# Kernel optimization log

Hardware: AMD Instinct MI355X
Metric: run time of the kernel (lower is better)

## Reference

```python
import jax, jax.numpy as jnp
import numpy as np

S, B, C, H, E, V, T = 196, 64, 1024, 1024, 512, 32000, 20


def setup_inputs() -> dict:
    key = jax.random.key(0)
    ks = jax.random.split(key, 16)

    def w(k, shape, fan_in):
        return (jax.random.normal(k, shape, jnp.float32) / np.sqrt(fan_in)).astype(jnp.float32)

    emb_W = w(ks[2], (V, E), E).at[0].set(0.0)  # padding_idx=0
    return {
        'ctx': jax.random.normal(ks[0], (S, B, C), jnp.float32),
        'y': jax.random.randint(ks[1], (T, B), 0, V, jnp.int32),
        'emb_W': emb_W,
        'att_ctx2ctx': w(ks[3], (C, C), C),
        'att_hid2ctx': w(ks[4], (H, C), H),
        'att_mlp': w(ks[5], (C,), C),
        'gru_W_ih': w(ks[6], (3 * H, E + C), E + C),
        'gru_b_ih': jnp.zeros((3 * H,), jnp.float32),
        'gru_W_hh': w(ks[7], (3 * H, H), H),
        'gru_b_hh': jnp.zeros((3 * H,), jnp.float32),
        'hid2out_W': w(ks[8], (E, H), H),
        'hid2out_b': jnp.zeros((E,), jnp.float32),
        'out_ctx_W': w(ks[9], (E, C), C),
        'out_ctx_b': jnp.zeros((E,), jnp.float32),
        'out2prob_W': w(ks[10], (V, E), E),
        'out2prob_b': jnp.zeros((V,), jnp.float32),
    }


def reference(ctx, y, emb_W, att_ctx2ctx, att_hid2ctx, att_mlp,
              gru_W_ih, gru_b_ih, gru_W_hh, gru_b_hh,
              hid2out_W, hid2out_b, out_ctx_W, out_ctx_b,
              out2prob_W, out2prob_b):
    hidden = gru_W_hh.shape[1]
    y_emb = emb_W[y]                                        # [T, B, E]
    ctx_proj = jnp.einsum('sbc,cm->sbm', ctx, att_ctx2ctx)  # precompute ctx2ctx(ctx)

    def gru_cell(x, h):
        gi = x @ gru_W_ih.T + gru_b_ih
        gh = h @ gru_W_hh.T + gru_b_hh
        i_r, i_z, i_n = jnp.split(gi, 3, axis=-1)
        h_r, h_z, h_n = jnp.split(gh, 3, axis=-1)
        r = jax.nn.sigmoid(i_r + h_r)
        z = jax.nn.sigmoid(i_z + h_z)
        n = jnp.tanh(i_n + r * h_n)
        return (1.0 - z) * n + z * h

    def step(h, inp):
        y_t, tgt = inp                                      # [B,E], [B]
        # MLP attention over source positions S
        scores = jnp.einsum('sbm,m->sb', jnp.tanh(ctx_proj + (h @ att_hid2ctx)[None]), att_mlp)
        alpha = jax.nn.softmax(scores, axis=0)              # [S, B]
        z_t = jnp.einsum('sb,sbc->bc', alpha, ctx)          # [B, C]
        ht = gru_cell(jnp.concatenate([y_t, z_t], axis=-1), h)
        logit = jnp.tanh(ht @ hid2out_W.T + hid2out_b)      # hid2out (tanh FF)
        logit = logit + y_t                                 # prev2out
        logit = logit + z_t @ out_ctx_W.T + out_ctx_b       # ctx2out
        log_p = jax.nn.log_softmax(jnp.tanh(logit) @ out2prob_W.T + out2prob_b, axis=-1)
        mask = (tgt != 0).astype(log_p.dtype)               # NLLLoss ignore_index=0, sum
        nll = -jnp.sum(jnp.take_along_axis(log_p, tgt[:, None], axis=1)[:, 0] * mask)
        return ht, nll

    h0 = jnp.zeros((y.shape[1], hidden), ctx.dtype)         # dec_init='zero'
    _, nlls = jax.lax.scan(step, h0, (y_emb[:-1], y[1:]))
    return jnp.sum(nlls)
```

## Files before the change

### kernel.cpp

```cpp
#include <hip/hip_runtime.h>
#include <math.h>

#define TS_ 19

typedef float f32x4 __attribute__((ext_vector_type(4)));
typedef short s16x8 __attribute__((ext_vector_type(8)));
typedef unsigned short us;
typedef unsigned char uc;

__device__ __forceinline__ float sigmoidf_(float x) { return 1.f / (1.f + __expf(-x)); }

__device__ __forceinline__ float fast_tanh(float x) {
    float ax = fabsf(x);
    float e = __expf(-2.f * ax);
    float r = (1.f - e) * __builtin_amdgcn_rcpf(1.f + e);
    return copysignf(r, x);
}

__device__ __forceinline__ us f2b(float x) {
    union { float f; unsigned u; } v; v.f = x;
    unsigned r = v.u + 0x7fffu + ((v.u >> 16) & 1u);
    return (us)(r >> 16);
}
__device__ __forceinline__ float b2f(us u) {
    union { unsigned u; float f; } v; v.u = ((unsigned)u) << 16; return v.f;
}
__device__ __forceinline__ uc f2e4m3(float x) {
    return (uc)(__builtin_amdgcn_cvt_pk_fp8_f32(x, 0.f, 0, false) & 0xff);
}

#define MFMA(a, b, c) __builtin_amdgcn_mfma_f32_16x16x32_bf16((a), (b), (c), 0, 0, 0)
#define MFMA8(a, b, c) __builtin_amdgcn_mfma_f32_16x16x32_fp8_fp8((a), (b), (c), 0, 0, 0)

__device__ __forceinline__ f32x4 zero4() { return (f32x4){0.f, 0.f, 0.f, 0.f}; }

__device__ __forceinline__ f32x4 wg16(const us* ap, const us* bp, int nk, f32x4 acc) {
#pragma unroll 4
    for (int k = 0; k < nk; k += 32)
        acc = MFMA(*(const s16x8*)(ap + k), *(const s16x8*)(bp + k), acc);
    return acc;
}

__device__ __forceinline__ void gload_lds16(const void* g, void* l) {
    __builtin_amdgcn_global_load_lds(
        (const __attribute__((address_space(1))) unsigned int*)g,
        (__attribute__((address_space(3))) unsigned int*)l, 16, 0, 0);
}

__global__ __launch_bounds__(256) void k_prep(
    const float* __restrict__ ctx, us* __restrict__ ctxbf,
    const float* __restrict__ o2pW, uc* __restrict__ o2p8,
    const float* __restrict__ Wih, const float* __restrict__ Whh, us* __restrict__ Wg,
    const float* __restrict__ h2oW, us* __restrict__ h2obf,
    const float* __restrict__ octxW, us* __restrict__ octxbf,
    const float* __restrict__ att_c2c, us* __restrict__ c2cT,
    const float* __restrict__ att_h2c, us* __restrict__ attbf,
    const int* __restrict__ y, const float* __restrict__ embW, us* __restrict__ xc,
    float* __restrict__ hf32, us* __restrict__ ht_all,
    us* __restrict__ obf_all, uc* __restrict__ obf8, float* __restrict__ out) {
    __shared__ float tile[32][33];
    int bid = blockIdx.x, tid = threadIdx.x;
    const int4 z4 = {0, 0, 0, 0};

    if (bid < 1024) {
        for (long i = ((long)bid * 256 + tid) * 4; i < 12845056L; i += 1048576L) {
            float4 v = *(const float4*)(ctx + i);
            ushort4 o = { f2b(v.x), f2b(v.y), f2b(v.z), f2b(v.w) };
            *(ushort4*)(ctxbf + i) = o;
        }
    } else if (bid < 1792) {
        for (long i = ((long)(bid - 1024) * 256 + tid) * 8; i < 16384000L;
             i += 1572864L) {
            float4 v0 = *(const float4*)(o2pW + i);
            float4 v1 = *(const float4*)(o2pW + i + 4);
            int lo = __builtin_amdgcn_cvt_pk_fp8_f32(v0.x, v0.y, 0, false);
            lo = __builtin_amdgcn_cvt_pk_fp8_f32(v0.z, v0.w, lo, true);
            int hi = __builtin_amdgcn_cvt_pk_fp8_f32(v1.x, v1.y, 0, false);
            hi = __builtin_amdgcn_cvt_pk_fp8_f32(v1.z, v1.w, hi, true);
            int2 o = { lo, hi };
            *(int2*)(o2p8 + i) = o;
        }
    } else if (bid < 2816) {
        for (int n = bid - 1792; n < 4096; n += 1024) {
            int cl = n >> 10;
            if (cl < 2) {
                long bb = (long)n * 2560;
                const float* wi = Wih + (long)n * 1536;
                const float* wh = Whh + (long)n * 1024;
                for (int k = tid; k < 1536; k += 256) Wg[bb + k] = f2b(wi[k]);
                for (int k = tid; k < 1024; k += 256) Wg[bb + 1536 + k] = f2b(wh[k]);
            } else if (cl == 2) {
                long bb = 5242880L + (long)(n - 2048) * 1536;
                const float* wi = Wih + (long)n * 1536;
                for (int k = tid; k < 1536; k += 256) Wg[bb + k] = f2b(wi[k]);
            } else {
                long bb = 6815744L + (long)(n - 3072) * 1024;
                const float* wh = Whh + (long)(n - 1024) * 1024;
                for (int k = tid; k < 1024; k += 256) Wg[bb + k] = f2b(wh[k]);
            }
        }
    } else if (bid < 2880) {
        for (long i = ((long)(bid - 2816) * 256 + tid) * 4; i < 524288L; i += 65536L) {
            float4 v = *(const float4*)(h2oW + i);
            ushort4 o = { f2b(v.x), f2b(v.y), f2b(v.z), f2b(v.w) };
            *(ushort4*)(h2obf + i) = o;
        }
    } else if (bid < 2944) {
        for (long i = ((long)(bid - 2880) * 256 + tid) * 4; i < 524288L; i += 65536L) {
            float4 v = *(const float4*)(octxW + i);
            ushort4 o = { f2b(v.x), f2b(v.y), f2b(v.z), f2b(v.w) };
            *(ushort4*)(octxbf + i) = o;
        }
    } else if (bid < 3072) {
        for (int r = bid - 2944; r < 1216; r += 128) {
            int row = y[r];
            const float* src = embW + (long)row * 512;
            us* dst = xc + (long)r * 2560;
            for (int e = tid; e < 512; e += 256) dst[e] = f2b(src[e]);
        }
    } else if (bid < 4096) {
        int g = bid - 3072;
        int bx = (g & 31) * 32, by = (g >> 5) * 32;
        int x = tid & 31, y0 = tid >> 5;
        for (int yy = y0; yy < 32; yy += 8) tile[yy][x] = att_c2c[(by + yy) * 1024 + bx + x];
        __syncthreads();
        for (int yy = y0; yy < 32; yy += 8) c2cT[(bx + yy) * 1024 + by + x] = f2b(tile[x][yy]);
    } else if (bid < 5120) {
        int g = bid - 4096;
        int bx = (g & 31) * 32, by = (g >> 5) * 32;
        int x = tid & 31, y0 = tid >> 5;
        for (int yy = y0; yy < 32; yy += 8) tile[yy][x] = att_h2c[(by + yy) * 1024 + bx + x];
        __syncthreads();
        for (int yy = y0; yy < 32; yy += 8) attbf[(bx + yy) * 1024 + by + x] = f2b(tile[x][yy]);
    } else {
        int zb = bid - 5120;
        if (zb < 32) {
            int4* p = (int4*)hf32;
            int i = zb * 256 + tid;
            p[i] = z4; p[i + 8192] = z4;
        } else if (zb < 40) {
            int4* p = (int4*)ht_all;
            int i = (zb - 32) * 256 + tid;
#pragma unroll
            for (int k = 0; k < 4; ++k) p[i + k * 2048] = z4;
        } else if (zb < 56) {
            int cbase = (zb - 40) * 4;
#pragma unroll
            for (int c = 0; c < 4; ++c) {
                ushort4* p = (ushort4*)(xc + (long)(cbase + c) * 2560 + 1536);
                ushort4 o = {0, 0, 0, 0};
                p[tid] = o;
            }
        } else if (zb < 64) {
            int4* p = (int4*)(obf_all + 1216L * 512);
            int i = (zb - 56) * 256 + tid;
            p[i] = z4; p[i + 2048] = z4;
        } else if (zb < 68) {
            int4* p = (int4*)(obf8 + 1216L * 512);
            int i = (zb - 64) * 256 + tid;
            p[i] = z4; p[i + 1024] = z4;
        } else if (zb < 92) {
            int4* p = (int4*)(o2p8 + 16384000L);
            int i = (zb - 68) * 256 + tid;
#pragma unroll
            for (int k = 0; k < 4; ++k) p[i + k * 6144] = z4;
        } else {
            if (tid == 0) out[0] = 0.f;
        }
    }
}

__global__ __launch_bounds__(256) void k_gemm(const us* __restrict__ A,
                                              const us* __restrict__ Bt,
                                              us* __restrict__ Cb) {
    __shared__ us As[8192], Bs[8192];
    int tid = threadIdx.x, lane = tid & 63, w = tid >> 6;
    int mr = lane & 15, kb = lane >> 4;
    int bm = blockIdx.x % 98, bn = blockIdx.x / 98;
    long m0 = (long)bm * 128;
    int n0 = bn * 128;
    int wr = w >> 1, wc = w & 1;
    int srow = w * 32 + (lane >> 3);
    int ib = (lane & 7) * 16;

    f32x4 acc[4][4];
#pragma unroll
    for (int i = 0; i < 4; i++)
#pragma unroll
        for (int j = 0; j < 4; j++) acc[i][j] = zero4();

    for (int kt = 0; kt < 16; ++kt) {
        int k0 = kt * 64;
        __syncthreads();
#pragma unroll
        for (int c = 0; c < 4; ++c) {
            int r = srow + c * 8;
            int sw = (ib ^ ((r & 7) << 4)) >> 1;
            gload_lds16(A + (m0 + r) * 1024 + k0 + sw, &As[w * 2048 + c * 512]);
            gload_lds16(Bt + (long)(n0 + r) * 1024 + k0 + sw, &Bs[w * 2048 + c * 512]);
        }
        __syncthreads();
#pragma unroll
        for (int ks = 0; ks < 2; ++ks) {
            s16x8 af[4], bf[4];
#pragma unroll
            for (int mt = 0; mt < 4; ++mt) {
                int r = wr * 64 + mt * 16 + mr;
                af[mt] = *(const s16x8*)&As[(r * 128 + ((ks * 64 + kb * 16) ^ ((r & 7) << 4))) >> 1];
            }
#pragma unroll
            for (int nt = 0; nt < 4; ++nt) {
                int r = wc * 64 + nt * 16 + mr;
                bf[nt] = *(const s16x8*)&Bs[(r * 128 + ((ks * 64 + kb * 16) ^ ((r & 7) << 4))) >> 1];
            }
#pragma unroll
            for (int mt = 0; mt < 4; ++mt)
#pragma unroll
                for (int nt = 0; nt < 4; ++nt)
                    acc[mt][nt] = MFMA(af[mt], bf[nt], acc[mt][nt]);
        }
    }
#pragma unroll
    for (int mt = 0; mt < 4; ++mt)
#pragma unroll
        for (int nt = 0; nt < 4; ++nt)
#pragma unroll
            for (int j = 0; j < 4; ++j)
                Cb[(m0 + wr * 64 + mt * 16 + kb * 4 + j) * 1024 +
                   n0 + wc * 64 + nt * 16 + mr] = f2b(acc[mt][nt][j]);
}

__global__ __launch_bounds__(256) void k_hproj(const us* __restrict__ hcur,
                                               const us* __restrict__ attbf,
                                               float* __restrict__ hpp) {
    int tid = threadIdx.x, lane = tid & 63, w = tid >> 6;
    int vn0 = (blockIdx.x >> 1) * 16, kc = blockIdx.x & 1;
    int m0 = w * 16, mr = lane & 15, kb = lane >> 4;
    const us* ap = hcur + (long)(m0 + mr) * 1024 + kc * 512 + kb * 8;
    const us* bp = attbf + (long)(vn0 + mr) * 1024 + kc * 512 + kb * 8;
    f32x4 acc = wg16(ap, bp, 512, zero4());
#pragma unroll
    for (int j = 0; j < 4; ++j)
        hpp[(long)kc * 65536 + (long)(m0 + kb * 4 + j) * 1024 + vn0 + mr] = acc[j];
}

__global__ __launch_bounds__(1024) void k_scores(const us* __restrict__ cpb,
                                                 const float* __restrict__ hpp,
                                                 const float* __restrict__ mlp,
                                                 float* __restrict__ scores) {
    __shared__ float hp[1024];
    __shared__ float ml[1024];
    int tid = threadIdx.x;
    int b = blockIdx.x >> 2, sq = blockIdx.x & 3;
    hp[tid] = hpp[(long)b * 1024 + tid] + hpp[65536 + (long)b * 1024 + tid];
    ml[tid] = mlp[tid];
    __syncthreads();
    int wv = tid >> 6, lane = tid & 63;
    int s0 = sq * 49;
    for (int s = s0 + wv; s < s0 + 49; s += 16) {
        const us* cp = cpb + (long)(s * 64 + b) * 1024 + lane * 16;
        s16x8 c0 = *(const s16x8*)cp;
        s16x8 c1 = *(const s16x8*)(cp + 8);
        int e0 = lane * 16;
        float acc = 0.f;
#pragma unroll
        for (int j = 0; j < 8; ++j)
            acc += fast_tanh(b2f((us)c0[j]) + hp[e0 + j]) * ml[e0 + j];
#pragma unroll
        for (int j = 0; j < 8; ++j)
            acc += fast_tanh(b2f((us)c1[j]) + hp[e0 + 8 + j]) * ml[e0 + 8 + j];
#pragma unroll
        for (int off = 32; off; off >>= 1) acc += __shfl_xor(acc, off, 64);
        if (lane == 0) scores[b * 196 + s] = acc;
    }
}

__global__ __launch_bounds__(512) void k_z(const float* __restrict__ scores,
                                           const us* __restrict__ ctxbf,
                                           us* __restrict__ xc, int t) {
    __shared__ float red[512];
    __shared__ float als[196];
    __shared__ float zp[256];
    int tid = threadIdx.x, b = blockIdx.x >> 2, ch = blockIdx.x & 3;
    const float* sc = scores + b * 196;
    float lm = (tid < 196) ? sc[tid] : -1e30f;
    red[tid] = lm; __syncthreads();
    for (int st = 256; st; st >>= 1) { if (tid < st) red[tid] = fmaxf(red[tid], red[tid + st]); __syncthreads(); }
    float m = red[0]; __syncthreads();
    float ls = (tid < 196) ? __expf(sc[tid] - m) : 0.f;
    red[tid] = ls; __syncthreads();
    for (int st = 256; st; st >>= 1) { if (tid < st) red[tid] += red[tid + st]; __syncthreads(); }
    float inv = 1.f / red[0];
    if (tid < 196) als[tid] = ls * inv;
    __syncthreads();
    int c = ch * 256 + (tid & 255);
    int sh = tid >> 8;
    const us* cp = ctxbf + (long)b * 1024 + c;
    float a0 = 0.f;
    int sb = sh * 98;
#pragma unroll 4
    for (int s = sb; s < sb + 98; s += 2) {
        a0 += als[s] * b2f(cp[(long)s * 65536]) +
              als[s + 1] * b2f(cp[(long)(s + 1) * 65536]);
    }
    if (sh) zp[tid & 255] = a0;
    __syncthreads();
    if (!sh) {
        a0 += zp[tid & 255];
        xc[(long)(t * 64 + b) * 2560 + 512 + c] = f2b(a0);
    }
}

__global__ __launch_bounds__(512) void k_gruh2(us* __restrict__ xc,
                                               const us* __restrict__ Wg,
                                               const float* __restrict__ bih,
                                               const float* __restrict__ bhh,
                                               float* __restrict__ hf32,
                                               us* __restrict__ ht_all, int t) {
    __shared__ float lg[2048];
    int tid = threadIdx.x, lane = tid & 63, w = tid >> 6;
    int mr = lane & 15, kb = lane >> 4;
    int g = w >> 1, kh = w & 1;
    int xcd = blockIdx.x & 7, idx = blockIdx.x >> 3;
    int jt = xcd * 8 + (idx >> 2), mq = idx & 3;
    int m0 = mq * 16, j0 = jt * 16;
    const us* xr = xc + (long)t * 163840 + (long)(m0 + mr) * 2560;

    f32x4 acc = zero4();
    if (g == 0) {
        acc = wg16(xr + kh * 1280 + kb * 8,
                   Wg + (long)(j0 + mr) * 2560 + kh * 1280 + kb * 8, 1280, acc);
    } else if (g == 1) {
        acc = wg16(xr + kh * 1280 + kb * 8,
                   Wg + (long)(1024 + j0 + mr) * 2560 + kh * 1280 + kb * 8, 1280, acc);
    } else if (g == 2) {
        acc = wg16(xr + kh * 768 + kb * 8,
                   Wg + 5242880L + (long)(j0 + mr) * 1536 + kh * 768 + kb * 8, 768, acc);
    } else {
        acc = wg16(xr + 1536 + kh * 512 + kb * 8,
                   Wg + 6815744L + (long)(j0 + mr) * 1024 + kh * 512 + kb * 8, 512, acc);
    }
#pragma unroll
    for (int j = 0; j < 4; ++j)
        lg[(g * 2 + kh) * 256 + (kb * 4 + j) * 16 + mr] = acc[j];
    __syncthreads();

    if (tid < 256) {
        int ml = tid >> 4, jj = tid & 15;
        int b = m0 + ml, j = j0 + jj;
        float gr = lg[0 * 256 + ml * 16 + jj] + lg[1 * 256 + ml * 16 + jj];
        float gz = lg[2 * 256 + ml * 16 + jj] + lg[3 * 256 + ml * 16 + jj];
        float gi = lg[4 * 256 + ml * 16 + jj] + lg[5 * 256 + ml * 16 + jj];
        float gh = lg[6 * 256 + ml * 16 + jj] + lg[7 * 256 + ml * 16 + jj];
        float r  = sigmoidf_(gr + bih[j] + bhh[j]);
        float zz = sigmoidf_(gz + bih[1024 + j] + bhh[1024 + j]);
        float n  = fast_tanh(gi + bih[2048 + j] + r * (gh + bhh[2048 + j]));
        float h = (1.f - zz) * n + zz * hf32[b * 1024 + j];
        hf32[b * 1024 + j] = h;
        us hb = f2b(h);
        ht_all[(long)((t + 1) * 64 + b) * 1024 + j] = hb;
        if (t < TS_ - 1) xc[(long)((t + 1) * 64 + b) * 2560 + 1536 + j] = hb;
    }
}

__global__ __launch_bounds__(256) void k_outb(const us* __restrict__ ht_all,
                                              const us* __restrict__ xc,
                                              const us* __restrict__ h2obf,
                                              const float* __restrict__ h2ob,
                                              const us* __restrict__ octxbf,
                                              const float* __restrict__ octxb,
                                              us* __restrict__ obf_all,
                                              uc* __restrict__ obf8) {
    int tid = threadIdx.x, lane = tid & 63, w = tid >> 6;
    int mr = lane & 15, kb = lane >> 4;
    int m0 = blockIdx.x * 64;
    int n0 = blockIdx.y * 64;
    int e = n0 + w * 16 + mr;
    const us* bb1 = h2obf + (long)e * 1024 + kb * 8;
    const us* bb2 = octxbf + (long)e * 1024 + kb * 8;
    const us* ab1 = ht_all + (long)(64 + m0 + mr) * 1024 + kb * 8;
    const us* ab2 = xc + (long)(m0 + mr) * 2560 + 512 + kb * 8;

    f32x4 a1[4], a2[4];
#pragma unroll
    for (int i = 0; i < 4; i++) { a1[i] = zero4(); a2[i] = zero4(); }

#pragma unroll 2
    for (int k0 = 0; k0 < 1024; k0 += 32) {
        s16x8 b1 = *(const s16x8*)(bb1 + k0);
        s16x8 b2 = *(const s16x8*)(bb2 + k0);
#pragma unroll
        for (int mt = 0; mt < 4; ++mt) {
            a1[mt] = MFMA(*(const s16x8*)(ab1 + mt * 16384 + k0), b1, a1[mt]);
            a2[mt] = MFMA(*(const s16x8*)(ab2 + mt * 40960 + k0), b2, a2[mt]);
        }
    }
    float b1v = h2ob[e], b2v = octxb[e];
#pragma unroll
    for (int mt = 0; mt < 4; ++mt)
#pragma unroll
        for (int j = 0; j < 4; ++j) {
            long row = m0 + mt * 16 + kb * 4 + j;
            float ye = b2f(xc[row * 2560 + e]);
            float val = fast_tanh(fast_tanh(a1[mt][j] + b1v) + ye + a2[mt][j] + b2v);
            obf_all[(row << 9) + e] = f2b(val);
            obf8[(row << 9) + e] = f2e4m3(val);
        }
}

__global__ __launch_bounds__(256) void k_vocab8(const uc* __restrict__ obf8,
                                                const uc* __restrict__ o2p8,
                                                const float* __restrict__ o2pb,
                                                float* __restrict__ pm,
                                                float* __restrict__ ps) {
    __shared__ uc As[8192], Bs[8192];
    int tid = threadIdx.x, lane = tid & 63, w = tid >> 6;
    int mr = lane & 15, kb = lane >> 4;
    int xq = blockIdx.x & 7, idx = blockIdx.x >> 3;
    int nb = xq * 32 + idx / 10, mb = idx % 10;
    int m0 = mb * 128, n0 = nb * 128;
    int wr = w >> 1, wc = w & 1;
    int srow = w * 32 + (lane >> 2);
    int ib = (lane & 3) * 16;

    f32x4 acc[4][4];
#pragma unroll
    for (int i = 0; i < 4; i++)
#pragma unroll
        for (int j = 0; j < 4; j++) acc[i][j] = zero4();

    for (int kt = 0; kt < 8; ++kt) {
        int k0 = kt * 64;
        __syncthreads();
#pragma unroll
        for (int c = 0; c < 2; ++c) {
            int r = srow + c * 16;
            int sw = ib ^ ((r & 6) << 3);
            gload_lds16(obf8 + (long)(m0 + r) * 512 + k0 + sw, &As[w * 2048 + c * 1024]);
            gload_lds16(o2p8 + (long)(n0 + r) * 512 + k0 + sw, &Bs[w * 2048 + c * 1024]);
        }
        __syncthreads();
#pragma unroll
        for (int ks = 0; ks < 2; ++ks) {
            long af[4], bf[4];
#pragma unroll
            for (int mt = 0; mt < 4; ++mt) {
                int r = wr * 64 + mt * 16 + mr;
                af[mt] = *(const long*)&As[r * 64 + ((ks * 32 + kb * 8) ^ ((r & 6) << 3))];
            }
#pragma unroll
            for (int nt = 0; nt < 4; ++nt) {
                int r = wc * 64 + nt * 16 + mr;
                bf[nt] = *(const long*)&Bs[r * 64 + ((ks * 32 + kb * 8) ^ ((r & 6) << 3))];
            }
#pragma unroll
            for (int mt = 0; mt < 4; ++mt)
#pragma unroll
                for (int nt = 0; nt < 4; ++nt)
                    acc[mt][nt] = MFMA8(af[mt], bf[nt], acc[mt][nt]);
        }
    }

    int n0w = n0 + wc * 64;
    float bv[4];
#pragma unroll
    for (int nt = 0; nt < 4; ++nt) {
        int vn = n0w + nt * 16 + mr;
        bv[nt] = (vn < 32000) ? o2pb[vn] : -1e30f;
    }
#pragma unroll
    for (int mt = 0; mt < 4; ++mt)
#pragma unroll
        for (int j = 0; j < 4; ++j) {
            float x0 = acc[mt][0][j] + bv[0];
            float x1 = acc[mt][1][j] + bv[1];
            float x2 = acc[mt][2][j] + bv[2];
            float x3 = acc[mt][3][j] + bv[3];
            float m = fmaxf(fmaxf(x0, x1), fmaxf(x2, x3));
            float s = __expf(x0 - m) + __expf(x1 - m) + __expf(x2 - m) + __expf(x3 - m);
#pragma unroll
            for (int off = 1; off <= 8; off <<= 1) {
                float mo = __shfl_xor(m, off, 64), so = __shfl_xor(s, off, 64);
                float nm = fmaxf(m, mo);
                s = s * __expf(m - nm) + so * __expf(mo - nm);
                m = nm;
            }
            if (mr == 0) {
                int row = m0 + wr * 64 + mt * 16 + kb * 4 + j;
                pm[(long)(nb * 2 + wc) * 1280 + row] = m;
                ps[(long)(nb * 2 + wc) * 1280 + row] = s;
            }
        }
}

__global__ __launch_bounds__(64) void k_lseb(const float* __restrict__ pm,
                                             const float* __restrict__ ps,
                                             const us* __restrict__ obf_all,
                                             const float* __restrict__ o2pW,
                                             const float* __restrict__ o2pb,
                                             const int* __restrict__ y,
                                             float* __restrict__ out) {
    int r = blockIdx.x, lane = threadIdx.x;
    int t = r >> 6, b = r & 63;
    int tgt = y[(t + 1) * 64 + b];
    float m = -1e30f, s = 0.f;
    for (int p = lane; p < 512; p += 64) {
        float mi = pm[(long)p * 1280 + r], si = ps[(long)p * 1280 + r];
        float nm = fmaxf(m, mi);
        s = s * __expf(m - nm) + si * __expf(mi - nm);
        m = nm;
    }
#pragma unroll
    for (int off = 32; off; off >>= 1) {
        float mo = __shfl_xor(m, off, 64), so = __shfl_xor(s, off, 64);
        float nm = fmaxf(m, mo);
        s = s * __expf(m - nm) + so * __expf(mo - nm);
        m = nm;
    }
    float d = 0.f;
    const float* wr = o2pW + (long)tgt * 512;
#pragma unroll
    for (int k = 0; k < 8; ++k)
        d += b2f(obf_all[(long)r * 512 + lane + k * 64]) * wr[lane + k * 64];
#pragma unroll
    for (int off = 32; off; off >>= 1) d += __shfl_xor(d, off, 64);
    if (lane == 0 && tgt != 0)
        atomicAdd(out, (m + __logf(s)) - (d + o2pb[tgt]));
}

extern "C" void kernel_launch(void* const* d_in, const int* in_sizes, int n_in,
                              void* d_out, int out_size, void* d_ws, size_t ws_size,
                              hipStream_t stream) {
    const float* ctx     = (const float*)d_in[0];
    const int*   y       = (const int*)d_in[1];
    const float* embW    = (const float*)d_in[2];
    const float* att_c2c = (const float*)d_in[3];
    const float* att_h2c = (const float*)d_in[4];
    const float* mlp     = (const float*)d_in[5];
    const float* Wih     = (const float*)d_in[6];
    const float* bih     = (const float*)d_in[7];
    const float* Whh     = (const float*)d_in[8];
    const float* bhh     = (const float*)d_in[9];
    const float* h2oW    = (const float*)d_in[10];
    const float* h2ob    = (const float*)d_in[11];
    const float* octxW   = (const float*)d_in[12];
    const float* octxb   = (const float*)d_in[13];
    const float* o2pW    = (const float*)d_in[14];
    const float* o2pb    = (const float*)d_in[15];
    float* out = (float*)d_out;

    char* base = (char*)d_ws;
    us* ctxbf   = (us*)base; base += 25690112L;
    us* cpbf    = (us*)base; base += 25690112L;
    us* c2cT    = (us*)base; base += 2097152L;
    us* attbf   = (us*)base; base += 2097152L;
    us* Wg      = (us*)base; base += 15728640L;
    us* h2obf   = (us*)base; base += 1048576L;
    us* octxbf  = (us*)base; base += 1048576L;
    uc* o2p8    = (uc*)base; base += 16777216L;
    us* xc      = (us*)base; base += 6225920L;
    us* ht_all  = (us*)base; base += 2621440L;
    us* obf_all = (us*)base; base += 1310720L;
    uc* obf8    = (uc*)base; base += 655360L;
    float* hf32   = (float*)base; base += 262144L;
    float* hpp    = (float*)base; base += 524288L;
    float* scb    = (float*)base; base += 50176L;
    float* pm   = (float*)cpbf;
    float* ps   = pm + 655360L;

    k_prep<<<5213, 256, 0, stream>>>(ctx, ctxbf, o2pW, o2p8, Wih, Whh, Wg,
                                     h2oW, h2obf, octxW, octxbf,
                                     att_c2c, c2cT, att_h2c, attbf,
                                     y, embW, xc, hf32, ht_all, obf_all, obf8, out);
    k_gemm<<<784, 256, 0, stream>>>(ctxbf, c2cT, cpbf);

    for (int t = 0; t < TS_; t++) {
        k_hproj<<<128, 256, 0, stream>>>(ht_all + (long)t * 65536, attbf, hpp);
        k_scores<<<256, 1024, 0, stream>>>(cpbf, hpp, mlp, scb);
        k_z<<<256, 512, 0, stream>>>(scb, ctxbf, xc, t);
        k_gruh2<<<256, 512, 0, stream>>>(xc, Wg, bih, bhh, hf32, ht_all, t);
    }

    k_outb<<<dim3(19, 8), 256, 0, stream>>>(ht_all, xc, h2obf, h2ob, octxbf, octxb,
                                            obf_all, obf8);
    k_vocab8<<<2560, 256, 0, stream>>>(obf8, o2p8, o2pb, pm, ps);
    k_lseb<<<1216, 64, 0, stream>>>(pm, ps, obf_all, o2pW, o2pb, y, out);
}
```

Before: 982.7 us.

## Double-buffer LDS in fp8 vocab GEMM and vectorize GRU weight conversion

The fp8 vocab projection kernel now double-buffers its LDS tiles, prefetching the next K-slice with global_load_lds while MFMAs run on the current one, and uses one barrier per iteration instead of two. Separately, the GRU weight bf16 conversion in the prep kernel uses float4 vectorized loads and stores with half as many blocks, and the block ranges and grid size are shifted to match. The cost is doubled LDS use in the vocab kernel, which may reduce occupancy.

```diff
diff --git a/kernel.cpp b/kernel.cpp
--- a/kernel.cpp
+++ b/kernel.cpp
@@ -45,6 +45,12 @@
     __builtin_amdgcn_global_load_lds(
         (const __attribute__((address_space(1))) unsigned int*)g,
         (__attribute__((address_space(3))) unsigned int*)l, 16, 0, 0);
+}
+
+__device__ __forceinline__ void cvt4(const float* src, us* dst) {
+    float4 v = *(const float4*)src;
+    ushort4 o = { f2b(v.x), f2b(v.y), f2b(v.z), f2b(v.w) };
+    *(ushort4*)dst = o;
 }
 
 __global__ __launch_bounds__(256) void k_prep(
@@ -63,11 +69,8 @@
     const int4 z4 = {0, 0, 0, 0};
 
     if (bid < 1024) {
-        for (long i = ((long)bid * 256 + tid) * 4; i < 12845056L; i += 1048576L) {
-            float4 v = *(const float4*)(ctx + i);
-            ushort4 o = { f2b(v.x), f2b(v.y), f2b(v.z), f2b(v.w) };
-            *(ushort4*)(ctxbf + i) = o;
-        }
+        for (long i = ((long)bid * 256 + tid) * 4; i < 12845056L; i += 1048576L)
+            cvt4(ctx + i, ctxbf + i);
     } else if (bid < 1792) {
         for (long i = ((long)(bid - 1024) * 256 + tid) * 8; i < 16384000L;
              i += 1572864L) {
@@ -80,60 +83,55 @@
             int2 o = { lo, hi };
             *(int2*)(o2p8 + i) = o;
         }
-    } else if (bid < 2816) {
-        for (int n = bid - 1792; n < 4096; n += 1024) {
+    } else if (bid < 2304) {
+        for (int n = bid - 1792; n < 4096; n += 512) {
             int cl = n >> 10;
             if (cl < 2) {
-                long bb = (long)n * 2560;
+                us* wb = Wg + (long)n * 2560;
                 const float* wi = Wih + (long)n * 1536;
                 const float* wh = Whh + (long)n * 1024;
-                for (int k = tid; k < 1536; k += 256) Wg[bb + k] = f2b(wi[k]);
-                for (int k = tid; k < 1024; k += 256) Wg[bb + 1536 + k] = f2b(wh[k]);
+                for (int k4 = tid; k4 < 384; k4 += 256) cvt4(wi + k4 * 4, wb + k4 * 4);
+                if (tid < 256)
+                    cvt4(wh + tid * 4, wb + 1536 + tid * 4);
             } else if (cl == 2) {
-                long bb = 5242880L + (long)(n - 2048) * 1536;
+                us* wb = Wg + 5242880L + (long)(n - 2048) * 1536;
                 const float* wi = Wih + (long)n * 1536;
-                for (int k = tid; k < 1536; k += 256) Wg[bb + k] = f2b(wi[k]);
+                for (int k4 = tid; k4 < 384; k4 += 256) cvt4(wi + k4 * 4, wb + k4 * 4);
             } else {
-                long bb = 6815744L + (long)(n - 3072) * 1024;
+                us* wb = Wg + 6815744L + (long)(n - 3072) * 1024;
                 const float* wh = Whh + (long)(n - 1024) * 1024;
-                for (int k = tid; k < 1024; k += 256) Wg[bb + k] = f2b(wh[k]);
-            }
-        }
-    } else if (bid < 2880) {
-        for (long i = ((long)(bid - 2816) * 256 + tid) * 4; i < 524288L; i += 65536L) {
-            float4 v = *(const float4*)(h2oW + i);
-            ushort4 o = { f2b(v.x), f2b(v.y), f2b(v.z), f2b(v.w) };
-            *(ushort4*)(h2obf + i) = o;
-        }
-    } else if (bid < 2944) {
-        for (long i = ((long)(bid - 2880) * 256 + tid) * 4; i < 524288L; i += 65536L) {
-            float4 v = *(const float4*)(octxW + i);
-            ushort4 o = { f2b(v.x), f2b(v.y), f2b(v.z), f2b(v.w) };
-            *(ushort4*)(octxbf + i) = o;
-        }
-    } else if (bid < 3072) {
-        for (int r = bid - 2944; r < 1216; r += 128) {
+                cvt4(wh + tid * 4, wb + tid * 4);
+            }
+        }
+    } else if (bid < 2368) {
+        for (long i = ((long)(bid - 2304) * 256 + tid) * 4; i < 524288L; i += 65536L)
+            cvt4(h2oW + i, h2obf + i);
+    } else if (bid < 2432) {
+        for (long i = ((long)(bid - 2368) * 256 + tid) * 4; i < 524288L; i += 65536L)
+            cvt4(octxW + i, octxbf + i);
+    } else if (bid < 2560) {
+        for (int r = bid - 2432; r < 1216; r += 128) {
             int row = y[r];
             const float* src = embW + (long)row * 512;
             us* dst = xc + (long)r * 2560;
             for (int e = tid; e < 512; e += 256) dst[e] = f2b(src[e]);
         }
-    } else if (bid < 4096) {
-        int g = bid - 3072;
+    } else if (bid < 3584) {
+        int g = bid - 2560;
         int bx = (g & 31) * 32, by = (g >> 5) * 32;
         int x = tid & 31, y0 = tid >> 5;
         for (int yy = y0; yy < 32; yy += 8) tile[yy][x] = att_c2c[(by + yy) * 1024 + bx + x];
         __syncthreads();
         for (int yy = y0; yy < 32; yy += 8) c2cT[(bx + yy) * 1024 + by + x] = f2b(tile[x][yy]);
-    } else if (bid < 5120) {
-        int g = bid - 4096;
+    } else if (bid < 4608) {
+        int g = bid - 3584;
         int bx = (g & 31) * 32, by = (g >> 5) * 32;
         int x = tid & 31, y0 = tid >> 5;
         for (int yy = y0; yy < 32; yy += 8) tile[yy][x] = att_h2c[(by + yy) * 1024 + bx + x];
         __syncthreads();
         for (int yy = y0; yy < 32; yy += 8) attbf[(bx + yy) * 1024 + by + x] = f2b(tile[x][yy]);
     } else {
-        int zb = bid - 5120;
+        int zb = bid - 4608;
         if (zb < 32) {
             int4* p = (int4*)hf32;
             int i = zb * 256 + tid;
@@ -413,7 +411,7 @@
                                                 const float* __restrict__ o2pb,
                                                 float* __restrict__ pm,
                                                 float* __restrict__ ps) {
-    __shared__ uc As[8192], Bs[8192];
+    __shared__ uc As[2][8192], Bs[2][8192];
     int tid = threadIdx.x, lane = tid & 63, w = tid >> 6;
     int mr = lane & 15, kb = lane >> 4;
     int xq = blockIdx.x & 7, idx = blockIdx.x >> 3;
@@ -429,29 +427,41 @@
 #pragma unroll
         for (int j = 0; j < 4; j++) acc[i][j] = zero4();
 
+#pragma unroll
+    for (int c = 0; c < 2; ++c) {
+        int r = srow + c * 16;
+        int sw = ib ^ ((r & 6) << 3);
+        gload_lds16(obf8 + (long)(m0 + r) * 512 + sw, &As[0][w * 2048 + c * 1024]);
+        gload_lds16(o2p8 + (long)(n0 + r) * 512 + sw, &Bs[0][w * 2048 + c * 1024]);
+    }
+    __syncthreads();
+
+    int buf = 0;
     for (int kt = 0; kt < 8; ++kt) {
-        int k0 = kt * 64;
-        __syncthreads();
-#pragma unroll
-        for (int c = 0; c < 2; ++c) {
-            int r = srow + c * 16;
-            int sw = ib ^ ((r & 6) << 3);
-            gload_lds16(obf8 + (long)(m0 + r) * 512 + k0 + sw, &As[w * 2048 + c * 1024]);
-            gload_lds16(o2p8 + (long)(n0 + r) * 512 + k0 + sw, &Bs[w * 2048 + c * 1024]);
-        }
-        __syncthreads();
+        if (kt < 7) {
+            int k1 = (kt + 1) * 64;
+#pragma unroll
+            for (int c = 0; c < 2; ++c) {
+                int r = srow + c * 16;
+                int sw = ib ^ ((r & 6) << 3);
+                gload_lds16(obf8 + (long)(m0 + r) * 512 + k1 + sw,
+                            &As[buf ^ 1][w * 2048 + c * 1024]);
+                gload_lds16(o2p8 + (long)(n0 + r) * 512 + k1 + sw,
+                            &Bs[buf ^ 1][w * 2048 + c * 1024]);
+            }
+        }
 #pragma unroll
         for (int ks = 0; ks < 2; ++ks) {
             long af[4], bf[4];
 #pragma unroll
             for (int mt = 0; mt < 4; ++mt) {
                 int r = wr * 64 + mt * 16 + mr;
-                af[mt] = *(const long*)&As[r * 64 + ((ks * 32 + kb * 8) ^ ((r & 6) << 3))];
+                af[mt] = *(const long*)&As[buf][r * 64 + ((ks * 32 + kb * 8) ^ ((r & 6) << 3))];
             }
 #pragma unroll
             for (int nt = 0; nt < 4; ++nt) {
                 int r = wc * 64 + nt * 16 + mr;
-                bf[nt] = *(const long*)&Bs[r * 64 + ((ks * 32 + kb * 8) ^ ((r & 6) << 3))];
+                bf[nt] = *(const long*)&Bs[buf][r * 64 + ((ks * 32 + kb * 8) ^ ((r & 6) << 3))];
             }
 #pragma unroll
             for (int mt = 0; mt < 4; ++mt)
@@ -459,6 +469,8 @@
                 for (int nt = 0; nt < 4; ++nt)
                     acc[mt][nt] = MFMA8(af[mt], bf[nt], acc[mt][nt]);
         }
+        __syncthreads();
+        buf ^= 1;
     }
 
     int n0w = n0 + wc * 64;
@@ -568,7 +580,7 @@
     float* pm   = (float*)cpbf;
     float* ps   = pm + 655360L;
 
-    k_prep<<<5213, 256, 0, stream>>>(ctx, ctxbf, o2pW, o2p8, Wih, Whh, Wg,
+    k_prep<<<4701, 256, 0, stream>>>(ctx, ctxbf, o2pW, o2p8, Wih, Whh, Wg,
                                      h2oW, h2obf, octxW, octxbf,
                                      att_c2c, c2cT, att_h2c, attbf,
                                      y, embW, xc, hf32, ht_all, obf_all, obf8, out);
```

Measured after the change: 981.3 us (median of 2 runs). No clear change (-0.1%).
